# Kernel tuning notes

Hardware: AMD Instinct MI355X
Metric: run time of the kernel (lower is better)

The kernel has to match this reference:

```python
import jax, jax.numpy as jnp
import numpy as np

VOCAB_SIZE = 16384
BETA = 0.25
RESI_RATIO = 0.5  # abs(quant_resi=-0.5); kernel size 3


def setup_inputs() -> dict:
    key = jax.random.key(0)
    k1, k2, k3 = jax.random.split(key, 3)
    B, C, h, w = 16, 32, 32, 32
    f_BChw = jax.random.normal(k1, (B, C, h, w), dtype=jnp.float32)
    emb_weight = jax.random.normal(k2, (VOCAB_SIZE, C), dtype=jnp.float32)
    conv_w = jax.random.normal(k3, (C, C, 3, 3), dtype=jnp.float32) * 0.05
    conv_b = jnp.zeros((C,), dtype=jnp.float32)
    return {"f_BChw": f_BChw, "emb_weight": emb_weight, "conv_w": conv_w, "conv_b": conv_b}


def _res_conv(h_BChw, conv_w, conv_b):
    # ResConv: h*(1-r) + conv3x3(h)*r
    y = jax.lax.conv_general_dilated(
        h_BChw, conv_w, window_strides=(1, 1), padding=((1, 1), (1, 1)),
        dimension_numbers=("NCHW", "OIHW", "NCHW"))
    y = y + conv_b[None, :, None, None]
    return h_BChw * (1.0 - RESI_RATIO) + y * RESI_RATIO


def reference(f_BChw, emb_weight, conv_w, conv_b):
    f_BChw = f_BChw.astype(jnp.float32)
    B, C, h, w = f_BChw.shape
    query_NxC = jax.lax.stop_gradient(f_BChw).transpose(0, 2, 3, 1).reshape(-1, C)  # [N,C]
    # vocab_norm=False path: squared Euclidean distance via ||q||^2 + ||e||^2 - 2 q e^T
    E_dist = (jnp.sum(query_NxC * query_NxC, axis=1, keepdims=True)
              + jnp.sum(emb_weight * emb_weight, axis=1)
              - 2.0 * (query_NxC @ emb_weight.T))  # [N, vocab]
    idx_N = jnp.argmin(E_dist, axis=1)  # [N]
    # bincount for usage stats
    counts = jnp.zeros((VOCAB_SIZE,), dtype=jnp.float32).at[idx_N].add(1.0)
    # embedding gather -> [B,h,w,C] -> [B,C,h,w]
    zq_BChw = emb_weight[idx_N].reshape(B, h, w, C).transpose(0, 3, 1, 2)
    fhat_BChw = _res_conv(zq_BChw, conv_w, conv_b)
    vq_loss = (BETA * jnp.mean((jax.lax.stop_gradient(fhat_BChw) - f_BChw) ** 2)
               + jnp.mean((fhat_BChw - jax.lax.stop_gradient(f_BChw)) ** 2))
    # straight-through estimator
    fhat_out = f_BChw + jax.lax.stop_gradient(fhat_BChw - f_BChw)
    prob = counts / jnp.sum(counts)
    vocab_usage = jnp.mean((prob > 0.01 / VOCAB_SIZE).astype(jnp.float32)) * 100.0
    return fhat_out, vq_loss, vocab_usage
```

## Files before the change

### kernel.cpp

```cpp
#include <hip/hip_runtime.h>

#define VOCAB 16384
#define N_Q   16384
#define C     32
#define HW    1024
#define VCH   16
#define CODES_PER_CH 1024
#define TILES_PER_CH 64
#define GRP    8
#define NGRP   8
#define GBYTES 18432

typedef _Float16 half8 __attribute__((ext_vector_type(8)));
typedef float f32x4  __attribute__((ext_vector_type(4)));

__global__ __launch_bounds__(256) void k_prepE(const float* __restrict__ emb,
                                               float* __restrict__ enq,
                                               _Float16* __restrict__ hi, _Float16* __restrict__ lo,
                                               const float* __restrict__ convw,
                                               float* __restrict__ wp,
                                               unsigned long long* __restrict__ keys,
                                               int* __restrict__ counts) {
    int bx = blockIdx.x;
    if (bx >= 64) {
        if (bx == 64) {
            for (int k = threadIdx.x; k < C * C * 9; k += 256) {
                int cout = k / (C * 9);
                int r = k % (C * 9);
                int cin = r / 9;
                int tap = r % 9;
                wp[(tap * C + cin) * C + cout] = convw[k];
            }
        } else if (bx == 65) {
            for (int k = threadIdx.x; k < VOCAB; k += 256) keys[k] = ~0ULL;
        } else {
            for (int k = threadIdx.x; k < VOCAB; k += 256) counts[k] = 0;
        }
        return;
    }
    int j = bx * 256 + threadIdx.x;
    const float4* e4 = reinterpret_cast<const float4*>(emb + j * C);
    float s = 0.f;
    float v[C];
#pragma unroll
    for (int k = 0; k < 8; ++k) {
        float4 t = e4[k];
        v[4 * k] = t.x; v[4 * k + 1] = t.y; v[4 * k + 2] = t.z; v[4 * k + 3] = t.w;
        s += t.x * t.x + t.y * t.y + t.z * t.z + t.w * t.w;
    }
    float en2 = 0.5f * s;
    *reinterpret_cast<float4*>(enq + j * 4) = make_float4(en2, en2, en2, en2);
#pragma unroll
    for (int ko = 0; ko < 4; ++ko) {
        half8 vh, vl;
#pragma unroll
        for (int e = 0; e < 8; ++e) {
            float x = v[ko * 8 + e];
            _Float16 h = (_Float16)x;
            vh[e] = h;
            vl[e] = (_Float16)(x - (float)h);
        }
        int off = (j >> 4) * 512 + (((ko << 4) | (j & 15)) * 8);
        *reinterpret_cast<half8*>(hi + off) = vh;
        *reinterpret_cast<half8*>(lo + off) = vl;
    }
}

__device__ __forceinline__ void stage_grp(const char* ehib, const char* elob, const char* enqb,
                                          char* db, int chunk, int g, int w, int lane) {
#pragma unroll
    for (int k = 0; k < 5; ++k) {
        int widx = w + 4 * k;
        if (widx < 18) {
            const char* src;
            if (widx < 8)
                src = ehib + ((size_t)(chunk * TILES_PER_CH + g * GRP + widx) << 10);
            else if (widx < 16)
                src = elob + ((size_t)(chunk * TILES_PER_CH + g * GRP + widx - 8) << 10);
            else
                src = enqb + ((size_t)chunk * 16384 + (size_t)g * 2048 + (size_t)(widx - 16) * 1024);
            __builtin_amdgcn_global_load_lds(
                (const __attribute__((address_space(1))) void*)(src + lane * 16),
                (__attribute__((address_space(3))) void*)(db + widx * 1024 + lane * 16),
                16, 0, 0);
        }
    }
}

__global__ __attribute__((amdgpu_flat_work_group_size(256, 256), amdgpu_waves_per_eu(4, 4)))
void k_argmin(
    const float* __restrict__ f,
    const _Float16* __restrict__ Ehi, const _Float16* __restrict__ Elo,
    const float* __restrict__ enq,
    unsigned long long* __restrict__ keys) {
    __shared__ __align__(16) char lds[2 * GBYTES];
    int tid = threadIdx.x;
    int lane = tid & 63;
    int w = tid >> 6;
    int wid = blockIdx.x * 4 + w;
    int chunk = blockIdx.y;

    half8 a_hi[4], a_lo[4];
    int c0 = (lane >> 4) * 8;
#pragma unroll
    for (int qq = 0; qq < 4; ++qq) {
        int n = (wid * 4 + qq) * 16 + (lane & 15);
        int b = n >> 10, rem = n & 1023;
        const float* fp = f + (b * C + c0) * HW + rem;
#pragma unroll
        for (int e = 0; e < 8; ++e) {
            float x = -fp[e * HW];
            _Float16 h = (_Float16)x;
            a_hi[qq][e] = h;
            a_lo[qq][e] = (_Float16)(x - (float)h);
        }
    }

    float best[4][4];
    int   bt[4][4];
#pragma unroll
    for (int qq = 0; qq < 4; ++qq)
#pragma unroll
        for (int r = 0; r < 4; ++r) { best[qq][r] = 3.4e38f; bt[qq][r] = 0; }

    const char* ehib = (const char*)Ehi;
    const char* elob = (const char*)Elo;
    const char* enqb = (const char*)enq;

    stage_grp(ehib, elob, enqb, lds, chunk, 0, w, lane);
    __syncthreads();

    for (int g = 0; g < NGRP; ++g) {
        if (g + 1 < NGRP)
            stage_grp(ehib, elob, enqb, lds + ((g + 1) & 1) * GBYTES, chunk, g + 1, w, lane);
        const char* bb = lds + (g & 1) * GBYTES;
#pragma unroll
        for (int tt = 0; tt < GRP; ++tt) {
            half8 bh = *(const half8*)(bb + tt * 1024 + lane * 16);
            half8 bl = *(const half8*)(bb + 8192 + tt * 1024 + lane * 16);
            f32x4 eq = *(const f32x4*)(bb + 16384 + tt * 256 + (lane & 15) * 16);
#pragma unroll
            for (int qq = 0; qq < 4; ++qq) {
                f32x4 acc = __builtin_amdgcn_mfma_f32_16x16x32_f16(a_hi[qq], bh, eq, 0, 0, 0);
                acc = __builtin_amdgcn_mfma_f32_16x16x32_f16(a_hi[qq], bl, acc, 0, 0, 0);
                acc = __builtin_amdgcn_mfma_f32_16x16x32_f16(a_lo[qq], bh, acc, 0, 0, 0);
#pragma unroll
                for (int r = 0; r < 4; ++r) {
                    if (acc[r] < best[qq][r]) { best[qq][r] = acc[r]; bt[qq][r] = g * GRP + tt; }
                }
            }
        }
        __syncthreads();
    }

#pragma unroll
    for (int qq = 0; qq < 4; ++qq)
#pragma unroll
        for (int r = 0; r < 4; ++r) {
            float d = best[qq][r];
            int code = chunk * CODES_PER_CH + (bt[qq][r] << 4) + (lane & 15);
#pragma unroll
            for (int m = 1; m < 16; m <<= 1) {
                float od = __shfl_xor(d, m, 64);
                int oc = __shfl_xor(code, m, 64);
                if (od < d || (od == d && oc < code)) { d = od; code = oc; }
            }
            if ((lane & 15) == 0) {
                int row = ((lane >> 4) * 4) + r;
                int n = (wid * 4 + qq) * 16 + row;
                unsigned bits = __float_as_uint(d);
                unsigned s = ((int)bits >= 0) ? (bits | 0x80000000u) : ~bits;
                unsigned long long key = ((unsigned long long)s << 32) | (unsigned)code;
                atomicMin(&keys[n], key);
            }
        }
}

__global__ __launch_bounds__(256) void k_conv(const unsigned long long* __restrict__ keys,
                                              const float* __restrict__ emb,
                                              const float* __restrict__ wp,
                                              const float* __restrict__ bias,
                                              const float* __restrict__ f,
                                              int* __restrict__ counts,
                                              float* __restrict__ out,
                                              float* __restrict__ lpart) {
    __shared__ float sZ[128 * 33];
    __shared__ float sW[9216];
    __shared__ float red[256];
    int blk = blockIdx.x;
    int b = blk >> 4;
    int r0 = (blk & 15) * 2;
    int tid = threadIdx.x;

    {
        float4* dW = reinterpret_cast<float4*>(sW);
        const float4* sWp = reinterpret_cast<const float4*>(wp);
        for (int i = tid; i < 2304; i += 256) dW[i] = sWp[i];
    }
    {
        int px = tid >> 1, half = tid & 1;
        int row = px >> 5, col = px & 31;
        int gy = r0 - 1 + row;
        float* d = &sZ[px * 33 + half * 16];
        if (gy >= 0 && gy < 32) {
            int id = (int)(keys[b * HW + gy * 32 + col] & 0xFFFFFFFFULL);
            const float4* s = reinterpret_cast<const float4*>(emb + id * C + half * 16);
#pragma unroll
            for (int k = 0; k < 4; ++k) {
                float4 v = s[k];
                d[4 * k] = v.x; d[4 * k + 1] = v.y; d[4 * k + 2] = v.z; d[4 * k + 3] = v.w;
            }
        } else {
#pragma unroll
            for (int k = 0; k < 16; ++k) d[k] = 0.f;
        }
    }
    __syncthreads();

    int tx = tid & 31, ty = (tid >> 5) & 1, cg = tid >> 6;
    int co0 = cg * 8;
    int gy = r0 + ty;
    if (cg == 0) {
        int id = (int)(keys[b * HW + gy * 32 + tx] & 0xFFFFFFFFULL);
        atomicAdd(&counts[id], 1);
    }
    float acc[8];
#pragma unroll
    for (int u = 0; u < 8; ++u) acc[u] = bias[co0 + u];
    for (int dy = -1; dy <= 1; ++dy) {
        for (int dx = -1; dx <= 1; ++dx) {
            int gx = tx + dx;
            if (gx < 0 || gx >= 32) continue;
            const float* zp = &sZ[((ty + 1 + dy) * 32 + gx) * 33];
            int tap = (dy + 1) * 3 + (dx + 1);
            const float* wtap = &sW[tap * C * C + co0];
#pragma unroll
            for (int cin = 0; cin < C; ++cin) {
                float z = zp[cin];
                const f32x4* w4 = reinterpret_cast<const f32x4*>(wtap + cin * C);
                f32x4 wa = w4[0], wb = w4[1];
#pragma unroll
                for (int u = 0; u < 4; ++u) acc[u] = fmaf(z, wa[u], acc[u]);
#pragma unroll
                for (int u = 0; u < 4; ++u) acc[4 + u] = fmaf(z, wb[u], acc[4 + u]);
            }
        }
    }
    float lsum = 0.f;
#pragma unroll
    for (int u = 0; u < 8; ++u) {
        int cc = co0 + u;
        float zqv = sZ[((ty + 1) * 32 + tx) * 33 + cc];
        float fh = 0.5f * (zqv + acc[u]);
        int off = (b * C + cc) * HW + gy * 32 + tx;
        out[off] = fh;
        float diff = fh - f[off];
        lsum += diff * diff;
    }
    red[tid] = lsum;
    __syncthreads();
    for (int s = 128; s > 0; s >>= 1) {
        if (tid < s) red[tid] += red[tid + s];
        __syncthreads();
    }
    if (tid == 0) lpart[blk] = red[0];
}

__global__ __launch_bounds__(256) void k_final(const float* __restrict__ lpart,
                                               const int* __restrict__ counts,
                                               float* __restrict__ out) {
    __shared__ float red[256];
    __shared__ int redi[256];
    int tid = threadIdx.x;
    int used = 0;
    for (int i = tid; i < VOCAB; i += 256) used += (counts[i] != 0) ? 1 : 0;
    red[tid] = lpart[tid];
    redi[tid] = used;
    __syncthreads();
    for (int s = 128; s > 0; s >>= 1) {
        if (tid < s) { red[tid] += red[tid + s]; redi[tid] += redi[tid + s]; }
        __syncthreads();
    }
    if (tid == 0) {
        out[N_Q * C]     = 1.25f * red[0] / (float)(N_Q * C);
        out[N_Q * C + 1] = 100.f * (float)redi[0] / (float)VOCAB;
    }
}

extern "C" void kernel_launch(void* const* d_in, const int* in_sizes, int n_in,
                              void* d_out, int out_size, void* d_ws, size_t ws_size,
                              hipStream_t stream) {
    const float* f     = (const float*)d_in[0];
    const float* emb   = (const float*)d_in[1];
    const float* convw = (const float*)d_in[2];
    const float* convb = (const float*)d_in[3];
    float* out = (float*)d_out;
    float* ws  = (float*)d_ws;

    float*  wp     = ws;
    float*  lpart  = ws + 9216;
    int*    counts = (int*)(ws + 9472);
    unsigned long long* keys = (unsigned long long*)(ws + 25856);
    float*  enq    = ws + 58624;
    _Float16* Ehi  = (_Float16*)(ws + 124160);
    _Float16* Elo  = (_Float16*)(ws + 386304);

    k_prepE<<<67, 256, 0, stream>>>(emb, enq, Ehi, Elo, convw, wp, keys, counts);
    dim3 g2(64, VCH);
    k_argmin<<<g2, 256, 0, stream>>>(f, Ehi, Elo, enq, keys);
    k_conv<<<256, 256, 0, stream>>>(keys, emb, wp, convb, f, counts, out, lpart);
    k_final<<<1, 256, 0, stream>>>(lpart, counts, out);
}
```

Baseline: 91.94 us.

## Pack codebook into contiguous group blobs and fold argmin index into float bits

Rewrites the prep kernel to store hi, lo and half-norm data for each 8-tile group as one contiguous 18 KB blob, so staging into LDS uses a single base pointer instead of three address computations. The argmin loop packs the tile index into the low 6 mantissa bits of the distance and uses fminf, dropping the separate index registers and compare/select. Launch bounds change to allow 3 blocks per CU. Truncating mantissa bits slightly coarsens distance comparisons and can change tie-breaking between near-equal codes, and negative distances invert the ordering of the packed low bits.

```diff
diff --git a/kernel.cpp b/kernel.cpp
--- a/kernel.cpp
+++ b/kernel.cpp
@@ -15,8 +15,7 @@
 typedef float f32x4  __attribute__((ext_vector_type(4)));
 
 __global__ __launch_bounds__(256) void k_prepE(const float* __restrict__ emb,
-                                               float* __restrict__ enq,
-                                               _Float16* __restrict__ hi, _Float16* __restrict__ lo,
+                                               char* __restrict__ Eblob,
                                                const float* __restrict__ convw,
                                                float* __restrict__ wp,
                                                unsigned long long* __restrict__ keys,
@@ -49,7 +48,10 @@
         s += t.x * t.x + t.y * t.y + t.z * t.z + t.w * t.w;
     }
     float en2 = 0.5f * s;
-    *reinterpret_cast<float4*>(enq + j * 4) = make_float4(en2, en2, en2, en2);
+    int tg = j >> 4, G = tg >> 3, tt = tg & 7;
+    char* gb = Eblob + (size_t)G * GBYTES;
+    *reinterpret_cast<float4*>(gb + 16384 + tt * 256 + (j & 15) * 16)
+        = make_float4(en2, en2, en2, en2);
 #pragma unroll
     for (int ko = 0; ko < 4; ++ko) {
         half8 vh, vl;
@@ -60,38 +62,28 @@
             vh[e] = h;
             vl[e] = (_Float16)(x - (float)h);
         }
-        int off = (j >> 4) * 512 + (((ko << 4) | (j & 15)) * 8);
-        *reinterpret_cast<half8*>(hi + off) = vh;
-        *reinterpret_cast<half8*>(lo + off) = vl;
-    }
-}
-
-__device__ __forceinline__ void stage_grp(const char* ehib, const char* elob, const char* enqb,
-                                          char* db, int chunk, int g, int w, int lane) {
+        int lane = (ko << 4) | (j & 15);
+        *reinterpret_cast<half8*>(gb + tt * 1024 + lane * 16) = vh;
+        *reinterpret_cast<half8*>(gb + 8192 + tt * 1024 + lane * 16) = vl;
+    }
+}
+
+__device__ __forceinline__ void stage_grp(const char* gb, char* db, int w, int lane) {
 #pragma unroll
     for (int k = 0; k < 5; ++k) {
         int widx = w + 4 * k;
         if (widx < 18) {
-            const char* src;
-            if (widx < 8)
-                src = ehib + ((size_t)(chunk * TILES_PER_CH + g * GRP + widx) << 10);
-            else if (widx < 16)
-                src = elob + ((size_t)(chunk * TILES_PER_CH + g * GRP + widx - 8) << 10);
-            else
-                src = enqb + ((size_t)chunk * 16384 + (size_t)g * 2048 + (size_t)(widx - 16) * 1024);
             __builtin_amdgcn_global_load_lds(
-                (const __attribute__((address_space(1))) void*)(src + lane * 16),
+                (const __attribute__((address_space(1))) void*)(gb + widx * 1024 + lane * 16),
                 (__attribute__((address_space(3))) void*)(db + widx * 1024 + lane * 16),
                 16, 0, 0);
         }
     }
 }
 
-__global__ __attribute__((amdgpu_flat_work_group_size(256, 256), amdgpu_waves_per_eu(4, 4)))
-void k_argmin(
+__global__ __launch_bounds__(256, 3) void k_argmin(
     const float* __restrict__ f,
-    const _Float16* __restrict__ Ehi, const _Float16* __restrict__ Elo,
-    const float* __restrict__ enq,
+    const char* __restrict__ Eblob,
     unsigned long long* __restrict__ keys) {
     __shared__ __align__(16) char lds[2 * GBYTES];
     int tid = threadIdx.x;
@@ -117,28 +109,29 @@
     }
 
     float best[4][4];
-    int   bt[4][4];
 #pragma unroll
     for (int qq = 0; qq < 4; ++qq)
 #pragma unroll
-        for (int r = 0; r < 4; ++r) { best[qq][r] = 3.4e38f; bt[qq][r] = 0; }
-
-    const char* ehib = (const char*)Ehi;
-    const char* elob = (const char*)Elo;
-    const char* enqb = (const char*)enq;
-
-    stage_grp(ehib, elob, enqb, lds, chunk, 0, w, lane);
+        for (int r = 0; r < 4; ++r) best[qq][r] = __uint_as_float(0x7F800000u);
+
+    const char* gb0 = Eblob + (size_t)(chunk * NGRP) * GBYTES;
+
+    stage_grp(gb0, lds, w, lane);
     __syncthreads();
+
+    const char* bbl = lds + lane * 16;
+    const char* ebl = lds + 16384 + (lane & 15) * 16;
 
     for (int g = 0; g < NGRP; ++g) {
         if (g + 1 < NGRP)
-            stage_grp(ehib, elob, enqb, lds + ((g + 1) & 1) * GBYTES, chunk, g + 1, w, lane);
-        const char* bb = lds + (g & 1) * GBYTES;
+            stage_grp(gb0 + (size_t)(g + 1) * GBYTES, lds + ((g + 1) & 1) * GBYTES, w, lane);
+        int boff = (g & 1) * GBYTES;
 #pragma unroll
         for (int tt = 0; tt < GRP; ++tt) {
-            half8 bh = *(const half8*)(bb + tt * 1024 + lane * 16);
-            half8 bl = *(const half8*)(bb + 8192 + tt * 1024 + lane * 16);
-            f32x4 eq = *(const f32x4*)(bb + 16384 + tt * 256 + (lane & 15) * 16);
+            half8 bh = *(const half8*)(bbl + boff + tt * 1024);
+            half8 bl = *(const half8*)(bbl + boff + 8192 + tt * 1024);
+            f32x4 eq = *(const f32x4*)(ebl + boff + tt * 256);
+            unsigned t = (unsigned)(g * GRP + tt);
 #pragma unroll
             for (int qq = 0; qq < 4; ++qq) {
                 f32x4 acc = __builtin_amdgcn_mfma_f32_16x16x32_f16(a_hi[qq], bh, eq, 0, 0, 0);
@@ -146,7 +139,8 @@
                 acc = __builtin_amdgcn_mfma_f32_16x16x32_f16(a_lo[qq], bh, acc, 0, 0, 0);
 #pragma unroll
                 for (int r = 0; r < 4; ++r) {
-                    if (acc[r] < best[qq][r]) { best[qq][r] = acc[r]; bt[qq][r] = g * GRP + tt; }
+                    float pk = __uint_as_float((__float_as_uint(acc[r]) & 0xFFFFFFC0u) | t);
+                    best[qq][r] = fminf(best[qq][r], pk);
                 }
             }
         }
@@ -158,7 +152,8 @@
 #pragma unroll
         for (int r = 0; r < 4; ++r) {
             float d = best[qq][r];
-            int code = chunk * CODES_PER_CH + (bt[qq][r] << 4) + (lane & 15);
+            int t = (int)(__float_as_uint(d) & 63u);
+            int code = chunk * CODES_PER_CH + (t << 4) + (lane & 15);
 #pragma unroll
             for (int m = 1; m < 16; m <<= 1) {
                 float od = __shfl_xor(d, m, 64);
@@ -301,13 +296,11 @@
     float*  lpart  = ws + 9216;
     int*    counts = (int*)(ws + 9472);
     unsigned long long* keys = (unsigned long long*)(ws + 25856);
-    float*  enq    = ws + 58624;
-    _Float16* Ehi  = (_Float16*)(ws + 124160);
-    _Float16* Elo  = (_Float16*)(ws + 386304);
-
-    k_prepE<<<67, 256, 0, stream>>>(emb, enq, Ehi, Elo, convw, wp, keys, counts);
+    char*   Eblob  = (char*)(ws + 58624);
+
+    k_prepE<<<67, 256, 0, stream>>>(emb, Eblob, convw, wp, keys, counts);
     dim3 g2(64, VCH);
-    k_argmin<<<g2, 256, 0, stream>>>(f, Ehi, Elo, enq, keys);
+    k_argmin<<<g2, 256, 0, stream>>>(f, Eblob, keys);
     k_conv<<<256, 256, 0, stream>>>(keys, emb, wp, convb, f, counts, out, lpart);
     k_final<<<1, 256, 0, stream>>>(lpart, counts, out);
 }
```

Result: faster. 88.63 us (-3.6%).
